# Performance work log

Measured on AMD Instinct MI355X. Metric: run time of the kernel, lower is better.

The kernel has to match this reference:

```python
import jax, jax.numpy as jnp
import numpy as np

POSE_DIM, H_DIM, LATENT_DIM, NUM_LAYERS = 96, 32, 16, 2
BATCH, OBS_LEN, PRED_LEN = 16384, 16, 25


def setup_inputs() -> dict:
    key = jax.random.key(0)
    ks = jax.random.split(key, 16)
    s = 0.1
    inp = {
        "obs_s": jax.random.normal(ks[0], (OBS_LEN, BATCH, POSE_DIM), jnp.float32),
        "latent": jax.random.normal(ks[1], (BATCH, LATENT_DIM), jnp.float32),
        "pred_len": PRED_LEN,
        # FC: latent_dim -> h_dim
        "W_fc": jax.random.normal(ks[2], (H_DIM, LATENT_DIM), jnp.float32) * s,
        "b_fc": jnp.zeros((H_DIM,), jnp.float32),
        # LSTM layer 0 (input pose_dim), PyTorch gate order i,f,g,o
        "W_ih0": jax.random.normal(ks[3], (4 * H_DIM, POSE_DIM), jnp.float32) * s,
        "W_hh0": jax.random.normal(ks[4], (4 * H_DIM, H_DIM), jnp.float32) * s,
        "b_ih0": jax.random.normal(ks[5], (4 * H_DIM,), jnp.float32) * s,
        "b_hh0": jax.random.normal(ks[6], (4 * H_DIM,), jnp.float32) * s,
        # LSTM layer 1 (input h_dim)
        "W_ih1": jax.random.normal(ks[7], (4 * H_DIM, H_DIM), jnp.float32) * s,
        "W_hh1": jax.random.normal(ks[8], (4 * H_DIM, H_DIM), jnp.float32) * s,
        "b_ih1": jax.random.normal(ks[9], (4 * H_DIM,), jnp.float32) * s,
        "b_hh1": jax.random.normal(ks[10], (4 * H_DIM,), jnp.float32) * s,
        # mlp: h_dim -> pose_dim
        "W_mlp": jax.random.normal(ks[11], (POSE_DIM, H_DIM), jnp.float32) * s,
        "b_mlp": jnp.zeros((POSE_DIM,), jnp.float32),
    }
    return inp


def _lstm_cell(x, h, c, W_ih, W_hh, b):
    # x: [B, in], h/c: [B, H]; gates in PyTorch order i, f, g, o
    gates = x @ W_ih.T + h @ W_hh.T + b
    i, f, g, o = jnp.split(gates, 4, axis=-1)
    c_new = jax.nn.sigmoid(f) * c + jax.nn.sigmoid(i) * jnp.tanh(g)
    h_new = jax.nn.sigmoid(o) * jnp.tanh(c_new)
    return h_new, c_new


def reference(obs_s, latent, pred_len, W_fc, b_fc,
              W_ih0, W_hh0, b_ih0, b_hh0,
              W_ih1, W_hh1, b_ih1, b_hh1,
              W_mlp, b_mlp):
    batch = obs_s.shape[1]
    h_init = latent @ W_fc.T + b_fc                    # [B, H] -> both layers
    c0 = jnp.zeros((batch, H_DIM), obs_s.dtype)
    b0 = b_ih0 + b_hh0
    b1 = b_ih1 + b_hh1

    def step(carry, _):
        last, h0, c0_, h1, c1_ = carry
        h0, c0_ = _lstm_cell(last, h0, c0_, W_ih0, W_hh0, b0)
        h1, c1_ = _lstm_cell(h0, h1, c1_, W_ih1, W_hh1, b1)
        curr = h1 @ W_mlp.T + b_mlp                    # [B, pose_dim]
        return (curr, h0, c0_, h1, c1_), curr

    init = (obs_s[-1], h_init, c0, h_init, c0)
    _, preds = jax.lax.scan(step, init, None, length=pred_len)
    return preds  # [pred_len, B, pose_dim]
```

## Files before the change

kernel.cpp:

```cpp
#include <hip/hip_runtime.h>


#define PRED 25
#define BATCH 16384
#define EST   48

typedef unsigned short u16;
typedef unsigned int   u32;
typedef __attribute__((ext_vector_type(8))) short bf16x8;
typedef __attribute__((ext_vector_type(4))) float f32x4;

#define LOG2E  1.44269504088896340736f
#define LOG2E2 2.88539008177792681472f

__device__ __forceinline__ float rcp_(float x){ return __builtin_amdgcn_rcpf(x); }
__device__ __forceinline__ float ex2(float x){ return __builtin_amdgcn_exp2f(x); }
__device__ __forceinline__ float sigm2(float xp){ return rcp_(1.0f + ex2(-xp)); }
__device__ __forceinline__ float tanh2(float xp){ return 1.0f - 2.0f*rcp_(ex2(xp) + 1.0f); }

__device__ __forceinline__ u16 f2b(float f){
  u32 i = __float_as_uint(f);
  i += 0x7FFFu + ((i >> 16) & 1u);
  return (u16)(i >> 16);
}
__device__ __forceinline__ float b2f(u16 u){ return __uint_as_float(((u32)u) << 16); }

__device__ __forceinline__ float act_h(f32x4 g, float& c){
  float ig = sigm2(g[0]);
  float fg = sigm2(g[1]);
  float gg = tanh2(g[2]);
  float og = sigm2(g[3]);
  c = fmaf(fg, c, ig*gg);
  return og * tanh2(c*LOG2E2);
}

extern "C" __global__ void prep_kernel(const float* __restrict__ Wih0,
                                       const float* __restrict__ Wmlp,
                                       const float* __restrict__ bih0,
                                       const float* __restrict__ bhh0,
                                       const float* __restrict__ bmlp,
                                       float* __restrict__ ws){
  int idx = blockIdx.x*256 + threadIdx.x;
  if (idx < 4096){
    int g = idx >> 5, u = idx & 31;
    const float* wr = Wih0 + g*96;
    const float* wc = Wmlp + u;
    float a = 0.f;
    #pragma unroll 8
    for (int p = 0; p < 96; ++p) a = fmaf(wr[p], wc[p*32], a);
    ws[idx] = a;
  } else if (idx < 4224){
    int g = idx - 4096;
    const float* wr = Wih0 + g*96;
    float a = bih0[g] + bhh0[g];
    #pragma unroll 8
    for (int p = 0; p < 96; ++p) a = fmaf(wr[p], bmlp[p], a);
    ws[idx] = a;
  }
}

struct __align__(16) SM {
  u16 h0[32*EST];
  u16 h1h[32*EST];
  u16 h1lo[32*EST];
};

extern "C" __global__ __launch_bounds__(128, 1)
void decoder_kernel(const float* __restrict__ obs,  const float* __restrict__ lat,
                    const float* __restrict__ Wfc,  const float* __restrict__ bfc,
                    const float* __restrict__ Wih0, const float* __restrict__ Whh0,
                    const float* __restrict__ bih0, const float* __restrict__ bhh0,
                    const float* __restrict__ Wih1, const float* __restrict__ Whh1,
                    const float* __restrict__ bih1, const float* __restrict__ bhh1,
                    const float* __restrict__ Wmlp, const float* __restrict__ bmlp,
                    const float* __restrict__ ws,   float* __restrict__ out)
{
  __shared__ SM sm;
  const int tid = threadIdx.x;
  const int mh  = tid >> 6;
  const int l   = tid & 63;
  const int lr  = l & 15;
  const int kq  = l >> 4;
  const int ebase = blockIdx.x * 32;

  for (int v = tid; v < 32*EST; v += 128) sm.h1lo[v] = 0;
  for (int v = tid; v < 1024; v += 128){
    int e = v >> 5, u = v & 31;
    const float* lp = lat + (size_t)(ebase + e)*16;
    const float* wf = Wfc + u*16;
    float a = bfc[u];
    #pragma unroll
    for (int p = 0; p < 16; ++p) a = fmaf(wf[p], lp[p], a);
    sm.h1h[e*EST + (u&3)*8 + (u>>2)] = f2b(a);
  }

  bf16x8 wcombf[4], whh0f[4], wih1f[4], whh1f[4];
  #pragma unroll
  for (int i = 0; i < 4; ++i){
    int vg = (mh*4 + i)*16 + lr;
    int g  = (vg & 3)*32 + (vg >> 2);
    float sc = ((vg & 3) == 2) ? LOG2E2 : LOG2E;
    union{bf16x8 v; u16 s[8];} a, b, c, d;
    #pragma unroll
    for (int j = 0; j < 8; ++j){
      int col = 4*j + kq;
      a.s[j] = f2b(ws[g*32 + col]*sc);
      b.s[j] = f2b(Whh0[g*32 + col]*sc);
      c.s[j] = f2b(Wih1[g*32 + col]*sc);
      d.s[j] = f2b(Whh1[g*32 + col]*sc);
    }
    wcombf[i] = a.v; whh0f[i] = b.v; wih1f[i] = c.v; whh1f[i] = d.v;
  }
  bf16x8 awm[3];
  #pragma unroll
  for (int im = 0; im < 3; ++im){
    int o = (mh*3 + im)*16 + lr;
    union{bf16x8 v; u16 s[8];} fr;
    #pragma unroll
    for (int j = 0; j < 8; ++j) fr.s[j] = f2b(Wmlp[o*32 + 4*j + kq]);
    awm[im] = fr.v;
  }
  f32x4 bcombr[4], b1r[4];
  #pragma unroll
  for (int i = 0; i < 4; ++i){
    int u = (mh*4 + i)*4 + kq;
    #pragma unroll
    for (int r = 0; r < 4; ++r){
      int g = r*32 + u;
      float sc = (r == 2) ? LOG2E2 : LOG2E;
      bcombr[i][r] = ws[4096 + g]*sc;
      b1r[i][r]    = (bih1[g] + bhh1[g])*sc;
    }
  }
  f32x4 bmv[3];
  #pragma unroll
  for (int im = 0; im < 3; ++im){
    int o0 = (mh*3 + im)*16 + kq*4;
    #pragma unroll
    for (int r = 0; r < 4; ++r) bmv[im][r] = bmlp[o0 + r];
  }

  float c0a[2][4] = {{0,0,0,0},{0,0,0,0}};
  float c1a[2][4] = {{0,0,0,0},{0,0,0,0}};

  __syncthreads();

  bf16x8 h1hfrag[2];
  #pragma unroll
  for (int s = 0; s < 2; ++s)
    h1hfrag[s] = *(const bf16x8*)&sm.h1h[(16*s + lr)*EST + kq*8];

  {
    bf16x8 bx[2][3];
    #pragma unroll
    for (int s = 0; s < 2; ++s){
      const float* xr = obs + ((size_t)15*BATCH + ebase + 16*s + lr)*96;
      #pragma unroll
      for (int c = 0; c < 3; ++c){
        union{bf16x8 v; u16 q[8];} fr;
        const float* s8 = xr + c*32 + kq*8;
        #pragma unroll
        for (int j = 0; j < 8; ++j) fr.q[j] = f2b(s8[j]);
        bx[s][c] = fr.v;
      }
    }
    #pragma unroll
    for (int i = 0; i < 4; ++i){
      int vg = (mh*4 + i)*16 + lr;
      int g  = (vg & 3)*32 + (vg >> 2);
      float sc = ((vg & 3) == 2) ? LOG2E2 : LOG2E;
      bf16x8 wf[3];
      #pragma unroll
      for (int c = 0; c < 3; ++c){
        union{bf16x8 v; u16 q[8];} fr;
        const float* s8 = Wih0 + g*96 + c*32 + kq*8;
        #pragma unroll
        for (int j = 0; j < 8; ++j) fr.q[j] = f2b(s8[j]*sc);
        wf[c] = fr.v;
      }
      int u = (mh*4 + i)*4 + kq;
      f32x4 b00;
      #pragma unroll
      for (int r = 0; r < 4; ++r){
        int gg = r*32 + u;
        b00[r] = (bih0[gg] + bhh0[gg])*((r == 2) ? LOG2E2 : LOG2E);
      }
      #pragma unroll
      for (int s = 0; s < 2; ++s){
        f32x4 acc = b00;
        acc = __builtin_amdgcn_mfma_f32_16x16x32_bf16(wf[0], bx[s][0], acc, 0, 0, 0);
        acc = __builtin_amdgcn_mfma_f32_16x16x32_bf16(wf[1], bx[s][1], acc, 0, 0, 0);
        acc = __builtin_amdgcn_mfma_f32_16x16x32_bf16(wf[2], bx[s][2], acc, 0, 0, 0);
        acc = __builtin_amdgcn_mfma_f32_16x16x32_bf16(whh0f[i], h1hfrag[s], acc, 0, 0, 0);
        float h = act_h(acc, c0a[s][i]);
        sm.h0[(16*s + lr)*EST + kq*8 + mh*4 + i] = f2b(h);
      }
    }
  }
  __syncthreads();

  #pragma unroll 1
  for (int t = 0; t < PRED; ++t){
    bf16x8 h0frag[2];
    #pragma unroll
    for (int s = 0; s < 2; ++s)
      h0frag[s] = *(const bf16x8*)&sm.h0[(16*s + lr)*EST + kq*8];
    #pragma unroll
    for (int s = 0; s < 2; ++s){
      union{u16 q[4]; u32 w[2];} hi4, lo4;
      #pragma unroll
      for (int i = 0; i < 4; ++i){
        f32x4 acc = b1r[i];
        acc = __builtin_amdgcn_mfma_f32_16x16x32_bf16(wih1f[i], h0frag[s], acc, 0, 0, 0);
        acc = __builtin_amdgcn_mfma_f32_16x16x32_bf16(whh1f[i], h1hfrag[s], acc, 0, 0, 0);
        float h = act_h(acc, c1a[s][i]);
        u16 hb = f2b(h);
        hi4.q[i] = hb;
        lo4.q[i] = f2b(h - b2f(hb));
      }
      int base = (16*s + lr)*EST + kq*8 + mh*4;
      *(u32*)&sm.h1h[base]      = hi4.w[0];
      *(u32*)&sm.h1h[base + 2]  = hi4.w[1];
      *(u32*)&sm.h1lo[base]     = lo4.w[0];
      *(u32*)&sm.h1lo[base + 2] = lo4.w[1];
    }
    __syncthreads();
    bf16x8 h1lofrag[2];
    #pragma unroll
    for (int s = 0; s < 2; ++s){
      h1hfrag[s]  = *(const bf16x8*)&sm.h1h[(16*s + lr)*EST + kq*8];
      h1lofrag[s] = *(const bf16x8*)&sm.h1lo[(16*s + lr)*EST + kq*8];
    }
    if (t < PRED-1){
      #pragma unroll
      for (int s = 0; s < 2; ++s){
        union{u16 q[4]; u32 w[2];} h4;
        #pragma unroll
        for (int i = 0; i < 4; ++i){
          f32x4 acc = bcombr[i];
          acc = __builtin_amdgcn_mfma_f32_16x16x32_bf16(wcombf[i], h1hfrag[s], acc, 0, 0, 0);
          acc = __builtin_amdgcn_mfma_f32_16x16x32_bf16(whh0f[i],  h0frag[s],  acc, 0, 0, 0);
          float h = act_h(acc, c0a[s][i]);
          h4.q[i] = f2b(h);
        }
        int base = (16*s + lr)*EST + kq*8 + mh*4;
        *(u32*)&sm.h0[base]     = h4.w[0];
        *(u32*)&sm.h0[base + 2] = h4.w[1];
      }
    }
    #pragma unroll
    for (int s = 0; s < 2; ++s){
      float* ob = out + (size_t)t*BATCH*96 + (size_t)(ebase + 16*s + lr)*96;
      #pragma unroll
      for (int im = 0; im < 3; ++im){
        f32x4 acc = bmv[im];
        acc = __builtin_amdgcn_mfma_f32_16x16x32_bf16(awm[im], h1hfrag[s],  acc, 0, 0, 0);
        acc = __builtin_amdgcn_mfma_f32_16x16x32_bf16(awm[im], h1lofrag[s], acc, 0, 0, 0);
        *(f32x4*)(ob + (mh*3 + im)*16 + kq*4) = acc;
      }
    }
    if (t < PRED-1) __syncthreads();
  }
}

extern "C" void kernel_launch(void* const* d_in, const int* in_sizes, int n_in,
                              void* d_out, int out_size, void* d_ws, size_t ws_size,
                              hipStream_t stream){
  const float* obs  = (const float*)d_in[0];
  const float* lat  = (const float*)d_in[1];
  const float* Wfc  = (const float*)d_in[3];
  const float* bfc  = (const float*)d_in[4];
  const float* Wih0 = (const float*)d_in[5];
  const float* Whh0 = (const float*)d_in[6];
  const float* bih0 = (const float*)d_in[7];
  const float* bhh0 = (const float*)d_in[8];
  const float* Wih1 = (const float*)d_in[9];
  const float* Whh1 = (const float*)d_in[10];
  const float* bih1 = (const float*)d_in[11];
  const float* bhh1 = (const float*)d_in[12];
  const float* Wmlp = (const float*)d_in[13];
  const float* bmlp = (const float*)d_in[14];
  float* ws = (float*)d_ws;

  prep_kernel<<<dim3(17), dim3(256), 0, stream>>>(Wih0, Wmlp, bih0, bhh0, bmlp, ws);
  decoder_kernel<<<dim3(BATCH/32), dim3(128), 0, stream>>>(
      obs, lat, Wfc, bfc, Wih0, Whh0, bih0, bhh0,
      Wih1, Whh1, bih1, bhh1, Wmlp, bmlp, ws, (float*)d_out);
}
```

Measured before the change: 83.07 us.

## Double-buffer swizzled LDS hidden state and use LDS-only barriers in LSTM loop

Replaces the padded h0/h1-hi/h1-lo LDS arrays with a single swizzled, ping-pong buffered hidden-state layout and a permuted K ordering. The barrier waits only on LDS counters, so global output stores are not drained at each sync. The bf16 hi/lo split for h1 in the output MLP is dropped, halving those MFMAs but lowering output precision. Uses native bf16 conversion and 64-bit packed LDS stores.

Result: faster. 72.97 us (-12.2%).

```diff
diff --git a/kernel.cpp b/kernel.cpp
--- a/kernel.cpp
+++ b/kernel.cpp
@@ -3,15 +3,19 @@
 
 #define PRED 25
 #define BATCH 16384
-#define EST   48
+#define ET    32
+#define HROW  128
 
 typedef unsigned short u16;
 typedef unsigned int   u32;
+typedef unsigned long long u64;
 typedef __attribute__((ext_vector_type(8))) short bf16x8;
 typedef __attribute__((ext_vector_type(4))) float f32x4;
 
 #define LOG2E  1.44269504088896340736f
 #define LOG2E2 2.88539008177792681472f
+
+#define BARRIER_NOVM() asm volatile("s_waitcnt lgkmcnt(0)\ns_barrier" ::: "memory")
 
 __device__ __forceinline__ float rcp_(float x){ return __builtin_amdgcn_rcpf(x); }
 __device__ __forceinline__ float ex2(float x){ return __builtin_amdgcn_exp2f(x); }
@@ -19,19 +23,27 @@
 __device__ __forceinline__ float tanh2(float xp){ return 1.0f - 2.0f*rcp_(ex2(xp) + 1.0f); }
 
 __device__ __forceinline__ u16 f2b(float f){
-  u32 i = __float_as_uint(f);
-  i += 0x7FFFu + ((i >> 16) & 1u);
-  return (u16)(i >> 16);
-}
-__device__ __forceinline__ float b2f(u16 u){ return __uint_as_float(((u32)u) << 16); }
-
-__device__ __forceinline__ float act_h(f32x4 g, float& c){
-  float ig = sigm2(g[0]);
-  float fg = sigm2(g[1]);
-  float gg = tanh2(g[2]);
-  float og = sigm2(g[3]);
-  c = fmaf(fg, c, ig*gg);
-  return og * tanh2(c*LOG2E2);
+  __bf16 b = (__bf16)f;
+  return __builtin_bit_cast(u16, b);
+}
+__device__ __forceinline__ u32 f2b2(float lo, float hi){
+  return (u32)f2b(lo) | ((u32)f2b(hi) << 16);
+}
+
+__device__ __forceinline__ int sperm(int v){
+  return (v & ~15) | ((v & 3) << 2) | ((v >> 2) & 3);
+}
+
+struct __align__(16) SM {
+  u16 hh[2][16*HROW];
+};
+__device__ __forceinline__ int swh(int e, int k){ return e*HROW + (k ^ ((e&7)<<3)); }
+
+__device__ __forceinline__ bf16x8 pack8p(const float* row32, int kq, float s){
+  union { bf16x8 v; u16 h[8]; } fr;
+  #pragma unroll
+  for (int j = 0; j < 8; ++j) fr.h[j] = f2b(row32[sperm(kq*8 + j)]*s);
+  return fr.v;
 }
 
 extern "C" __global__ void prep_kernel(const float* __restrict__ Wih0,
@@ -59,12 +71,6 @@
   }
 }
 
-struct __align__(16) SM {
-  u16 h0[32*EST];
-  u16 h1h[32*EST];
-  u16 h1lo[32*EST];
-};
-
 extern "C" __global__ __launch_bounds__(128, 1)
 void decoder_kernel(const float* __restrict__ obs,  const float* __restrict__ lat,
                     const float* __restrict__ Wfc,  const float* __restrict__ bfc,
@@ -77,21 +83,28 @@
 {
   __shared__ SM sm;
   const int tid = threadIdx.x;
-  const int mh  = tid >> 6;
-  const int l   = tid & 63;
-  const int lr  = l & 15;
-  const int kq  = l >> 4;
-  const int ebase = blockIdx.x * 32;
-
-  for (int v = tid; v < 32*EST; v += 128) sm.h1lo[v] = 0;
-  for (int v = tid; v < 1024; v += 128){
-    int e = v >> 5, u = v & 31;
-    const float* lp = lat + (size_t)(ebase + e)*16;
+  const int ebase = blockIdx.x * ET;
+  const int mh = tid >> 6;
+  const int l  = tid & 63;
+  const int lr = l & 15;
+  const int kq = l >> 4;
+
+  {
+    int u = tid & 31, e8 = (tid >> 5)*8;
     const float* wf = Wfc + u*16;
-    float a = bfc[u];
-    #pragma unroll
-    for (int p = 0; p < 16; ++p) a = fmaf(wf[p], lp[p], a);
-    sm.h1h[e*EST + (u&3)*8 + (u>>2)] = f2b(a);
+    float bb = bfc[u];
+    int sp = sperm(u);
+    #pragma unroll
+    for (int r = 0; r < 8; ++r){
+      int e = e8 + r, s = e >> 4, er = e & 15;
+      const float* lp = lat + (size_t)(ebase + e)*16;
+      float a = bb;
+      #pragma unroll
+      for (int j = 0; j < 16; ++j) a = fmaf(wf[j], lp[j], a);
+      u16 hb = f2b(a);
+      sm.hh[s][swh(er, 32 + sp)] = hb;
+      sm.hh[s][swh(er, 64 + sp)] = hb;
+    }
   }
 
   bf16x8 wcombf[4], whh0f[4], wih1f[4], whh1f[4];
@@ -100,25 +113,16 @@
     int vg = (mh*4 + i)*16 + lr;
     int g  = (vg & 3)*32 + (vg >> 2);
     float sc = ((vg & 3) == 2) ? LOG2E2 : LOG2E;
-    union{bf16x8 v; u16 s[8];} a, b, c, d;
-    #pragma unroll
-    for (int j = 0; j < 8; ++j){
-      int col = 4*j + kq;
-      a.s[j] = f2b(ws[g*32 + col]*sc);
-      b.s[j] = f2b(Whh0[g*32 + col]*sc);
-      c.s[j] = f2b(Wih1[g*32 + col]*sc);
-      d.s[j] = f2b(Whh1[g*32 + col]*sc);
-    }
-    wcombf[i] = a.v; whh0f[i] = b.v; wih1f[i] = c.v; whh1f[i] = d.v;
+    wcombf[i] = pack8p(ws   + g*32, kq, sc);
+    whh0f[i]  = pack8p(Whh0 + g*32, kq, sc);
+    wih1f[i]  = pack8p(Wih1 + g*32, kq, sc);
+    whh1f[i]  = pack8p(Whh1 + g*32, kq, sc);
   }
   bf16x8 awm[3];
   #pragma unroll
-  for (int im = 0; im < 3; ++im){
-    int o = (mh*3 + im)*16 + lr;
-    union{bf16x8 v; u16 s[8];} fr;
-    #pragma unroll
-    for (int j = 0; j < 8; ++j) fr.s[j] = f2b(Wmlp[o*32 + 4*j + kq]);
-    awm[im] = fr.v;
+  for (int i = 0; i < 3; ++i){
+    int o = (mh*3 + i)*16 + lr;
+    awm[i] = pack8p(Wmlp + o*32, kq, 1.0f);
   }
   f32x4 bcombr[4], b1r[4];
   #pragma unroll
@@ -132,28 +136,24 @@
       b1r[i][r]    = (bih1[g] + bhh1[g])*sc;
     }
   }
-  f32x4 bmv[3];
-  #pragma unroll
-  for (int im = 0; im < 3; ++im){
-    int o0 = (mh*3 + im)*16 + kq*4;
-    #pragma unroll
-    for (int r = 0; r < 4; ++r) bmv[im][r] = bmlp[o0 + r];
-  }
-
-  float c0a[2][4] = {{0,0,0,0},{0,0,0,0}};
-  float c1a[2][4] = {{0,0,0,0},{0,0,0,0}};
+  f32x4 biasmv[3];
+  #pragma unroll
+  for (int i = 0; i < 3; ++i){
+    int o0 = (mh*3 + i)*16 + kq*4;
+    #pragma unroll
+    for (int r = 0; r < 4; ++r) biasmv[i][r] = bmlp[o0 + r];
+  }
+
+  float c0s[2][4] = {{0,0,0,0},{0,0,0,0}};
+  float c1s[2][4] = {{0,0,0,0},{0,0,0,0}};
 
   __syncthreads();
 
-  bf16x8 h1hfrag[2];
-  #pragma unroll
-  for (int s = 0; s < 2; ++s)
-    h1hfrag[s] = *(const bf16x8*)&sm.h1h[(16*s + lr)*EST + kq*8];
-
   {
-    bf16x8 bx[2][3];
+    bf16x8 bhi[2], bx[2][3];
     #pragma unroll
     for (int s = 0; s < 2; ++s){
+      bhi[s] = *(const bf16x8*)&sm.hh[s][swh(lr, 32 + kq*8)];
       const float* xr = obs + ((size_t)15*BATCH + ebase + 16*s + lr)*96;
       #pragma unroll
       for (int c = 0; c < 3; ++c){
@@ -191,75 +191,93 @@
         acc = __builtin_amdgcn_mfma_f32_16x16x32_bf16(wf[0], bx[s][0], acc, 0, 0, 0);
         acc = __builtin_amdgcn_mfma_f32_16x16x32_bf16(wf[1], bx[s][1], acc, 0, 0, 0);
         acc = __builtin_amdgcn_mfma_f32_16x16x32_bf16(wf[2], bx[s][2], acc, 0, 0, 0);
-        acc = __builtin_amdgcn_mfma_f32_16x16x32_bf16(whh0f[i], h1hfrag[s], acc, 0, 0, 0);
-        float h = act_h(acc, c0a[s][i]);
-        sm.h0[(16*s + lr)*EST + kq*8 + mh*4 + i] = f2b(h);
-      }
-    }
-  }
-  __syncthreads();
-
-  #pragma unroll 1
+        acc = __builtin_amdgcn_mfma_f32_16x16x32_bf16(whh0f[i], bhi[s], acc, 0, 0, 0);
+        float ig = sigm2(acc[0]);
+        float fg = sigm2(acc[1]);
+        float gg = tanh2(acc[2]);
+        float og = sigm2(acc[3]);
+        float cn = fmaf(fg, c0s[s][i], ig*gg);
+        c0s[s][i] = cn;
+        sm.hh[s][swh(lr, 16*mh + 4*kq + i)] = f2b(og * tanh2(cn*LOG2E2));
+      }
+    }
+  }
+  BARRIER_NOVM();
+
+  f32x4 am[2][3];
+
   for (int t = 0; t < PRED; ++t){
-    bf16x8 h0frag[2];
+    const int p  = t & 1;
+    const int pn = p ^ 1;
+    bf16x8 bh0[2], bh1p[2];
+    #pragma unroll
+    for (int s = 0; s < 2; ++s){
+      bh0[s]  = *(const bf16x8*)&sm.hh[s][swh(lr, 32*p + kq*8)];
+      bh1p[s] = *(const bf16x8*)&sm.hh[s][swh(lr, 64 + 32*p + kq*8)];
+    }
+    #pragma unroll
+    for (int s = 0; s < 2; ++s){
+      float hv[4];
+      #pragma unroll
+      for (int i = 0; i < 4; ++i){
+        f32x4 a = b1r[i];
+        a = __builtin_amdgcn_mfma_f32_16x16x32_bf16(wih1f[i], bh0[s],  a, 0, 0, 0);
+        a = __builtin_amdgcn_mfma_f32_16x16x32_bf16(whh1f[i], bh1p[s], a, 0, 0, 0);
+        float ig = sigm2(a[0]);
+        float fg = sigm2(a[1]);
+        float gg = tanh2(a[2]);
+        float og = sigm2(a[3]);
+        float cn = fmaf(fg, c1s[s][i], ig*gg);
+        c1s[s][i] = cn;
+        hv[i] = og * tanh2(cn*LOG2E2);
+      }
+      u64 pk = (u64)f2b2(hv[0], hv[1]) | ((u64)f2b2(hv[2], hv[3]) << 32);
+      *(u64*)&sm.hh[s][swh(lr, 64 + 32*pn + 16*mh + 4*kq)] = pk;
+    }
+    BARRIER_NOVM();
+    bf16x8 bh1n[2];
     #pragma unroll
     for (int s = 0; s < 2; ++s)
-      h0frag[s] = *(const bf16x8*)&sm.h0[(16*s + lr)*EST + kq*8];
-    #pragma unroll
-    for (int s = 0; s < 2; ++s){
-      union{u16 q[4]; u32 w[2];} hi4, lo4;
-      #pragma unroll
-      for (int i = 0; i < 4; ++i){
-        f32x4 acc = b1r[i];
-        acc = __builtin_amdgcn_mfma_f32_16x16x32_bf16(wih1f[i], h0frag[s], acc, 0, 0, 0);
-        acc = __builtin_amdgcn_mfma_f32_16x16x32_bf16(whh1f[i], h1hfrag[s], acc, 0, 0, 0);
-        float h = act_h(acc, c1a[s][i]);
-        u16 hb = f2b(h);
-        hi4.q[i] = hb;
-        lo4.q[i] = f2b(h - b2f(hb));
-      }
-      int base = (16*s + lr)*EST + kq*8 + mh*4;
-      *(u32*)&sm.h1h[base]      = hi4.w[0];
-      *(u32*)&sm.h1h[base + 2]  = hi4.w[1];
-      *(u32*)&sm.h1lo[base]     = lo4.w[0];
-      *(u32*)&sm.h1lo[base + 2] = lo4.w[1];
-    }
-    __syncthreads();
-    bf16x8 h1lofrag[2];
-    #pragma unroll
-    for (int s = 0; s < 2; ++s){
-      h1hfrag[s]  = *(const bf16x8*)&sm.h1h[(16*s + lr)*EST + kq*8];
-      h1lofrag[s] = *(const bf16x8*)&sm.h1lo[(16*s + lr)*EST + kq*8];
-    }
+      bh1n[s] = *(const bf16x8*)&sm.hh[s][swh(lr, 64 + 32*pn + kq*8)];
+    #pragma unroll
+    for (int s = 0; s < 2; ++s)
+      #pragma unroll
+      for (int i = 0; i < 3; ++i){
+        f32x4 a = biasmv[i];
+        a = __builtin_amdgcn_mfma_f32_16x16x32_bf16(awm[i], bh1n[s], a, 0, 0, 0);
+        am[s][i] = a;
+      }
     if (t < PRED-1){
       #pragma unroll
       for (int s = 0; s < 2; ++s){
-        union{u16 q[4]; u32 w[2];} h4;
+        float hv[4];
         #pragma unroll
         for (int i = 0; i < 4; ++i){
-          f32x4 acc = bcombr[i];
-          acc = __builtin_amdgcn_mfma_f32_16x16x32_bf16(wcombf[i], h1hfrag[s], acc, 0, 0, 0);
-          acc = __builtin_amdgcn_mfma_f32_16x16x32_bf16(whh0f[i],  h0frag[s],  acc, 0, 0, 0);
-          float h = act_h(acc, c0a[s][i]);
-          h4.q[i] = f2b(h);
+          f32x4 a = bcombr[i];
+          a = __builtin_amdgcn_mfma_f32_16x16x32_bf16(wcombf[i], bh1n[s], a, 0, 0, 0);
+          a = __builtin_amdgcn_mfma_f32_16x16x32_bf16(whh0f[i],  bh0[s],  a, 0, 0, 0);
+          float ig = sigm2(a[0]);
+          float fg = sigm2(a[1]);
+          float gg = tanh2(a[2]);
+          float og = sigm2(a[3]);
+          float cn = fmaf(fg, c0s[s][i], ig*gg);
+          c0s[s][i] = cn;
+          hv[i] = og * tanh2(cn*LOG2E2);
         }
-        int base = (16*s + lr)*EST + kq*8 + mh*4;
-        *(u32*)&sm.h0[base]     = h4.w[0];
-        *(u32*)&sm.h0[base + 2] = h4.w[1];
-      }
-    }
+        u64 pk = (u64)f2b2(hv[0], hv[1]) | ((u64)f2b2(hv[2], hv[3]) << 32);
+        *(u64*)&sm.hh[s][swh(lr, 32*pn + 16*mh + 4*kq)] = pk;
+      }
+    }
+    BARRIER_NOVM();
     #pragma unroll
     for (int s = 0; s < 2; ++s){
-      float* ob = out + (size_t)t*BATCH*96 + (size_t)(ebase + 16*s + lr)*96;
-      #pragma unroll
-      for (int im = 0; im < 3; ++im){
-        f32x4 acc = bmv[im];
-        acc = __builtin_amdgcn_mfma_f32_16x16x32_bf16(awm[im], h1hfrag[s],  acc, 0, 0, 0);
-        acc = __builtin_amdgcn_mfma_f32_16x16x32_bf16(awm[im], h1lofrag[s], acc, 0, 0, 0);
-        *(f32x4*)(ob + (mh*3 + im)*16 + kq*4) = acc;
-      }
-    }
-    if (t < PRED-1) __syncthreads();
+      float* outb = out + (size_t)t*BATCH*96 + (size_t)(ebase + s*16 + lr)*96;
+      #pragma unroll
+      for (int i = 0; i < 3; ++i){
+        int o0 = (mh*3 + i)*16 + kq*4;
+        *(f32x4*)(outb + o0) = am[s][i];
+      }
+    }
   }
 }
 
@@ -283,7 +301,7 @@
   float* ws = (float*)d_ws;
 
   prep_kernel<<<dim3(17), dim3(256), 0, stream>>>(Wih0, Wmlp, bih0, bhh0, bmlp, ws);
-  decoder_kernel<<<dim3(BATCH/32), dim3(128), 0, stream>>>(
+  decoder_kernel<<<dim3(BATCH/ET), dim3(128), 0, stream>>>(
       obs, lat, Wfc, bfc, Wih0, Whh0, bih0, bhh0,
       Wih1, Whh1, bih1, bhh1, Wmlp, bmlp, ws, (float*)d_out);
 }
```
